# Optimization experiments

Measured on AMD Instinct MI355X. Metric: run time of the kernel, lower is better.

Reference implementation:

```python
import jax, jax.numpy as jnp
import numpy as np

B = 500_000
D = 128
L = 4


def setup_inputs() -> dict:
    key = jax.random.key(0)
    k1, k2 = jax.random.split(key)
    inputs = jax.random.normal(k1, (B, D), dtype=jnp.float32)
    # xavier_normal for [D,1] slices: std = sqrt(2/(D+1))
    std = float(np.sqrt(2.0 / (D + 1)))
    kernels = jax.random.normal(k2, (L, D, 1), dtype=jnp.float32) * std
    biases = jnp.zeros((L, D, 1), dtype=jnp.float32)
    return {"inputs": inputs, "kernels": kernels, "biases": biases}


def reference(inputs, kernels, biases):
    # inputs: [B, D]; kernels/biases: [L, D, 1]
    x0 = inputs  # [B, D]
    xl = x0
    for i in range(kernels.shape[0]):
        w = kernels[i, :, 0]  # [D]
        b = biases[i, :, 0]   # [D]
        xl_w = jnp.einsum('bd,d->b', xl, w)  # [B], scalar per sample
        xl = x0 * xl_w[:, None] + b + xl     # rank-1 cross + bias + residual
    return xl
```

## Files before the change

kernel.cpp:

```cpp
#include <hip/hip_runtime.h>


#define CN_D 128
#define CN_L 4

__global__ __launch_bounds__(256) void crossnet_kernel(
    const float* __restrict__ inputs,
    const float* __restrict__ kernels,
    const float* __restrict__ biases,
    float* __restrict__ out,
    int nrows)
{
    const int lane = threadIdx.x & 31;
    const int row_in_blk = threadIdx.x >> 5;
    const int rows_per_blk = blockDim.x >> 5;

    float4 w4[CN_L], b4[CN_L];
#pragma unroll
    for (int i = 0; i < CN_L; ++i) {
        w4[i] = ((const float4*)(kernels + i * CN_D))[lane];
        b4[i] = ((const float4*)(biases + i * CN_D))[lane];
    }

    for (long long row = (long long)blockIdx.x * rows_per_blk + row_in_blk;
         row < nrows;
         row += (long long)gridDim.x * rows_per_blk)
    {
        const float4* xp = (const float4*)(inputs + row * CN_D);
        float4 x = xp[lane];
        float4 xl = x;

#pragma unroll
        for (int i = 0; i < CN_L; ++i) {
            float p = xl.x * w4[i].x + xl.y * w4[i].y
                    + xl.z * w4[i].z + xl.w * w4[i].w;
            p += __shfl_xor(p, 1);
            p += __shfl_xor(p, 2);
            p += __shfl_xor(p, 4);
            p += __shfl_xor(p, 8);
            p += __shfl_xor(p, 16);
            xl.x = fmaf(x.x, p, xl.x + b4[i].x);
            xl.y = fmaf(x.y, p, xl.y + b4[i].y);
            xl.z = fmaf(x.z, p, xl.z + b4[i].z);
            xl.w = fmaf(x.w, p, xl.w + b4[i].w);
        }

        float4* op = (float4*)(out + row * CN_D);
        op[lane] = xl;
    }
}

extern "C" void kernel_launch(void* const* d_in, const int* in_sizes, int n_in,
                              void* d_out, int out_size, void* d_ws, size_t ws_size,
                              hipStream_t stream) {
    const float* inputs  = (const float*)d_in[0];
    const float* kernels = (const float*)d_in[1];
    const float* biases  = (const float*)d_in[2];
    float* out = (float*)d_out;

    const int nrows = in_sizes[0] / CN_D;

    const int block = 256;
    const int grid  = 4096;

    crossnet_kernel<<<grid, block, 0, stream>>>(inputs, kernels, biases, out, nrows);
}
```

Before: 418.1 us.

## Collapse cross layers algebraically, process two rows per group, nontemporal stores

Rewrites the recurrence as xl = a*x0 + beta. The scalar a comes from four independent dot products of x0 with each layer weight, combined with precomputed bias-weight terms c[i]. This removes the serial dependency between the per-layer shuffle reductions. Each 32-lane group now processes two rows per iteration to add independent loads and shuffles for latency hiding, and outputs use nontemporal stores. The algebra relies on xl staying a scalar multiple of x0 plus a constant vector, and may change floating-point rounding slightly.

```diff
diff --git a/kernel.cpp b/kernel.cpp
--- a/kernel.cpp
+++ b/kernel.cpp
@@ -3,6 +3,8 @@
 
 #define CN_D 128
 #define CN_L 4
+
+typedef float fvec4 __attribute__((ext_vector_type(4)));
 
 __global__ __launch_bounds__(256) void crossnet_kernel(
     const float* __restrict__ inputs,
@@ -12,8 +14,8 @@
     int nrows)
 {
     const int lane = threadIdx.x & 31;
-    const int row_in_blk = threadIdx.x >> 5;
-    const int rows_per_blk = blockDim.x >> 5;
+    const int grp_in_blk = threadIdx.x >> 5;
+    const int grps_per_blk = blockDim.x >> 5;
 
     float4 w4[CN_L], b4[CN_L];
 #pragma unroll
@@ -22,31 +24,84 @@
         b4[i] = ((const float4*)(biases + i * CN_D))[lane];
     }
 
-    for (long long row = (long long)blockIdx.x * rows_per_blk + row_in_blk;
-         row < nrows;
-         row += (long long)gridDim.x * rows_per_blk)
+    float c[CN_L];
+    float4 beta = make_float4(0.f, 0.f, 0.f, 0.f);
+#pragma unroll
+    for (int i = 0; i < CN_L; ++i) {
+        float p = beta.x * w4[i].x + beta.y * w4[i].y
+                + beta.z * w4[i].z + beta.w * w4[i].w;
+        p += __shfl_xor(p, 1);
+        p += __shfl_xor(p, 2);
+        p += __shfl_xor(p, 4);
+        p += __shfl_xor(p, 8);
+        p += __shfl_xor(p, 16);
+        c[i] = p;
+        beta.x += b4[i].x; beta.y += b4[i].y;
+        beta.z += b4[i].z; beta.w += b4[i].w;
+    }
+
+    const long long gsz = (long long)gridDim.x * grps_per_blk;
+
+    for (long long rowA = (long long)blockIdx.x * grps_per_blk + grp_in_blk;
+         rowA < nrows;
+         rowA += 2 * gsz)
     {
-        const float4* xp = (const float4*)(inputs + row * CN_D);
-        float4 x = xp[lane];
-        float4 xl = x;
+        const long long rowB = rowA + gsz;
+        const bool hasB = (rowB < nrows);
+        const long long rB = hasB ? rowB : rowA;
 
-#pragma unroll
-        for (int i = 0; i < CN_L; ++i) {
-            float p = xl.x * w4[i].x + xl.y * w4[i].y
-                    + xl.z * w4[i].z + xl.w * w4[i].w;
-            p += __shfl_xor(p, 1);
-            p += __shfl_xor(p, 2);
-            p += __shfl_xor(p, 4);
-            p += __shfl_xor(p, 8);
-            p += __shfl_xor(p, 16);
-            xl.x = fmaf(x.x, p, xl.x + b4[i].x);
-            xl.y = fmaf(x.y, p, xl.y + b4[i].y);
-            xl.z = fmaf(x.z, p, xl.z + b4[i].z);
-            xl.w = fmaf(x.w, p, xl.w + b4[i].w);
-        }
+        float4 xA = ((const float4*)(inputs + rowA * CN_D))[lane];
+        float4 xB = ((const float4*)(inputs + rB  * CN_D))[lane];
 
-        float4* op = (float4*)(out + row * CN_D);
-        op[lane] = xl;
+        float dA0 = xA.x*w4[0].x + xA.y*w4[0].y + xA.z*w4[0].z + xA.w*w4[0].w;
+        float dA1 = xA.x*w4[1].x + xA.y*w4[1].y + xA.z*w4[1].z + xA.w*w4[1].w;
+        float dA2 = xA.x*w4[2].x + xA.y*w4[2].y + xA.z*w4[2].z + xA.w*w4[2].w;
+        float dA3 = xA.x*w4[3].x + xA.y*w4[3].y + xA.z*w4[3].z + xA.w*w4[3].w;
+        float dB0 = xB.x*w4[0].x + xB.y*w4[0].y + xB.z*w4[0].z + xB.w*w4[0].w;
+        float dB1 = xB.x*w4[1].x + xB.y*w4[1].y + xB.z*w4[1].z + xB.w*w4[1].w;
+        float dB2 = xB.x*w4[2].x + xB.y*w4[2].y + xB.z*w4[2].z + xB.w*w4[2].w;
+        float dB3 = xB.x*w4[3].x + xB.y*w4[3].y + xB.z*w4[3].z + xB.w*w4[3].w;
+
+        dA0 += __shfl_xor(dA0, 1);  dA1 += __shfl_xor(dA1, 1);
+        dA2 += __shfl_xor(dA2, 1);  dA3 += __shfl_xor(dA3, 1);
+        dB0 += __shfl_xor(dB0, 1);  dB1 += __shfl_xor(dB1, 1);
+        dB2 += __shfl_xor(dB2, 1);  dB3 += __shfl_xor(dB3, 1);
+
+        dA0 += __shfl_xor(dA0, 2);  dA1 += __shfl_xor(dA1, 2);
+        dA2 += __shfl_xor(dA2, 2);  dA3 += __shfl_xor(dA3, 2);
+        dB0 += __shfl_xor(dB0, 2);  dB1 += __shfl_xor(dB1, 2);
+        dB2 += __shfl_xor(dB2, 2);  dB3 += __shfl_xor(dB3, 2);
+
+        dA0 += __shfl_xor(dA0, 4);  dA1 += __shfl_xor(dA1, 4);
+        dA2 += __shfl_xor(dA2, 4);  dA3 += __shfl_xor(dA3, 4);
+        dB0 += __shfl_xor(dB0, 4);  dB1 += __shfl_xor(dB1, 4);
+        dB2 += __shfl_xor(dB2, 4);  dB3 += __shfl_xor(dB3, 4);
+
+        dA0 += __shfl_xor(dA0, 8);  dA1 += __shfl_xor(dA1, 8);
+        dA2 += __shfl_xor(dA2, 8);  dA3 += __shfl_xor(dA3, 8);
+        dB0 += __shfl_xor(dB0, 8);  dB1 += __shfl_xor(dB1, 8);
+        dB2 += __shfl_xor(dB2, 8);  dB3 += __shfl_xor(dB3, 8);
+
+        dA0 += __shfl_xor(dA0, 16); dA1 += __shfl_xor(dA1, 16);
+        dA2 += __shfl_xor(dA2, 16); dA3 += __shfl_xor(dA3, 16);
+        dB0 += __shfl_xor(dB0, 16); dB1 += __shfl_xor(dB1, 16);
+        dB2 += __shfl_xor(dB2, 16); dB3 += __shfl_xor(dB3, 16);
+
+        float aA = 1.f, aB = 1.f;
+        aA = fmaf(aA, dA0 + 1.f, c[0]);  aB = fmaf(aB, dB0 + 1.f, c[0]);
+        aA = fmaf(aA, dA1 + 1.f, c[1]);  aB = fmaf(aB, dB1 + 1.f, c[1]);
+        aA = fmaf(aA, dA2 + 1.f, c[2]);  aB = fmaf(aB, dB2 + 1.f, c[2]);
+        aA = fmaf(aA, dA3 + 1.f, c[3]);  aB = fmaf(aB, dB3 + 1.f, c[3]);
+
+        fvec4 oA, oB;
+        oA.x = fmaf(aA, xA.x, beta.x);  oA.y = fmaf(aA, xA.y, beta.y);
+        oA.z = fmaf(aA, xA.z, beta.z);  oA.w = fmaf(aA, xA.w, beta.w);
+        oB.x = fmaf(aB, xB.x, beta.x);  oB.y = fmaf(aB, xB.y, beta.y);
+        oB.z = fmaf(aB, xB.z, beta.z);  oB.w = fmaf(aB, xB.w, beta.w);
+
+        __builtin_nontemporal_store(oA, (fvec4*)(out + rowA * CN_D) + lane);
+        if (hasB)
+            __builtin_nontemporal_store(oB, (fvec4*)(out + rowB * CN_D) + lane);
     }
 }
 
```

Result: slower. 439.6 us (+5.1%).

## Collapse cross layers into one scalar recurrence with DPP reductions and prefetch

Applied to the files above, without the earlier changes.

Rewrites the per-row computation using the fact that every layer's output equals a scalar times x0 plus a cumulative bias. The four dot products with x0 are computed independently, and constants from the bias terms are precomputed per thread. This removes the serial dependency between layer reductions. The kernel also uses 16-lane groups with DPP row reductions in place of shuffles and prefetches the next row. The workload is memory-bound, so the gain depends mainly on whether the prefetch and the different access pattern help bandwidth.

```diff
diff --git a/kernel.cpp b/kernel.cpp
--- a/kernel.cpp
+++ b/kernel.cpp
@@ -3,6 +3,19 @@
 
 #define CN_D 128
 #define CN_L 4
+
+template <int CTRL>
+__device__ __forceinline__ float dpp_radd(float x) {
+    int t = __builtin_amdgcn_update_dpp(0, __float_as_int(x), CTRL, 0xF, 0xF, true);
+    return x + __int_as_float(t);
+}
+__device__ __forceinline__ float row16_allreduce(float x) {
+    x = dpp_radd<0xB1>(x);
+    x = dpp_radd<0x4E>(x);
+    x = dpp_radd<0x124>(x);
+    x = dpp_radd<0x128>(x);
+    return x;
+}
 
 __global__ __launch_bounds__(256) void crossnet_kernel(
     const float* __restrict__ inputs,
@@ -11,42 +24,90 @@
     float* __restrict__ out,
     int nrows)
 {
-    const int lane = threadIdx.x & 31;
-    const int row_in_blk = threadIdx.x >> 5;
-    const int rows_per_blk = blockDim.x >> 5;
+    const int lane = threadIdx.x & 15;
+    const int grp  = threadIdx.x >> 4;
+    const int gpb  = blockDim.x >> 4;
 
-    float4 w4[CN_L], b4[CN_L];
+    float4 wlo[CN_L], whi[CN_L];
 #pragma unroll
     for (int i = 0; i < CN_L; ++i) {
-        w4[i] = ((const float4*)(kernels + i * CN_D))[lane];
-        b4[i] = ((const float4*)(biases + i * CN_D))[lane];
+        wlo[i] = ((const float4*)(kernels + i * CN_D))[lane];
+        whi[i] = ((const float4*)(kernels + i * CN_D))[lane + 16];
     }
 
-    for (long long row = (long long)blockIdx.x * rows_per_blk + row_in_blk;
-         row < nrows;
-         row += (long long)gridDim.x * rows_per_blk)
-    {
-        const float4* xp = (const float4*)(inputs + row * CN_D);
-        float4 x = xp[lane];
-        float4 xl = x;
+    float c[CN_L];
+    float4 blo = make_float4(0.f, 0.f, 0.f, 0.f);
+    float4 bhi = make_float4(0.f, 0.f, 0.f, 0.f);
+#pragma unroll
+    for (int i = 0; i < CN_L; ++i) {
+        float p = blo.x*wlo[i].x + blo.y*wlo[i].y + blo.z*wlo[i].z + blo.w*wlo[i].w
+                + bhi.x*whi[i].x + bhi.y*whi[i].y + bhi.z*whi[i].z + bhi.w*whi[i].w;
+        c[i] = row16_allreduce(p);
+        float4 t;
+        t = ((const float4*)(biases + i * CN_D))[lane];
+        blo.x += t.x; blo.y += t.y; blo.z += t.z; blo.w += t.w;
+        t = ((const float4*)(biases + i * CN_D))[lane + 16];
+        bhi.x += t.x; bhi.y += t.y; bhi.z += t.z; bhi.w += t.w;
+    }
 
-#pragma unroll
-        for (int i = 0; i < CN_L; ++i) {
-            float p = xl.x * w4[i].x + xl.y * w4[i].y
-                    + xl.z * w4[i].z + xl.w * w4[i].w;
-            p += __shfl_xor(p, 1);
-            p += __shfl_xor(p, 2);
-            p += __shfl_xor(p, 4);
-            p += __shfl_xor(p, 8);
-            p += __shfl_xor(p, 16);
-            xl.x = fmaf(x.x, p, xl.x + b4[i].x);
-            xl.y = fmaf(x.y, p, xl.y + b4[i].y);
-            xl.z = fmaf(x.z, p, xl.z + b4[i].z);
-            xl.w = fmaf(x.w, p, xl.w + b4[i].w);
-        }
+    const int stride = gridDim.x * gpb;
+    int row = blockIdx.x * gpb + grp;
+    if (row >= nrows) return;
 
-        float4* op = (float4*)(out + row * CN_D);
-        op[lane] = xl;
+    const float4* __restrict__ in4  = (const float4*)inputs;
+    float4* __restrict__       out4 = (float4*)out;
+
+    float4 xlo = in4[row * 32 + lane];
+    float4 xhi = in4[row * 32 + lane + 16];
+
+    while (true) {
+        const int rnext = row + stride;
+        const bool hasN = rnext < nrows;
+        const int rn = hasN ? rnext : row;
+        float4 nlo = in4[rn * 32 + lane];
+        float4 nhi = in4[rn * 32 + lane + 16];
+
+        float d0, d1, d2, d3;
+        d0 = xlo.x * wlo[0].x;                 d1 = xlo.x * wlo[1].x;
+        d2 = xlo.x * wlo[2].x;                 d3 = xlo.x * wlo[3].x;
+        d0 = fmaf(xlo.y, wlo[0].y, d0);        d1 = fmaf(xlo.y, wlo[1].y, d1);
+        d2 = fmaf(xlo.y, wlo[2].y, d2);        d3 = fmaf(xlo.y, wlo[3].y, d3);
+        d0 = fmaf(xlo.z, wlo[0].z, d0);        d1 = fmaf(xlo.z, wlo[1].z, d1);
+        d2 = fmaf(xlo.z, wlo[2].z, d2);        d3 = fmaf(xlo.z, wlo[3].z, d3);
+        d0 = fmaf(xlo.w, wlo[0].w, d0);        d1 = fmaf(xlo.w, wlo[1].w, d1);
+        d2 = fmaf(xlo.w, wlo[2].w, d2);        d3 = fmaf(xlo.w, wlo[3].w, d3);
+        d0 = fmaf(xhi.x, whi[0].x, d0);        d1 = fmaf(xhi.x, whi[1].x, d1);
+        d2 = fmaf(xhi.x, whi[2].x, d2);        d3 = fmaf(xhi.x, whi[3].x, d3);
+        d0 = fmaf(xhi.y, whi[0].y, d0);        d1 = fmaf(xhi.y, whi[1].y, d1);
+        d2 = fmaf(xhi.y, whi[2].y, d2);        d3 = fmaf(xhi.y, whi[3].y, d3);
+        d0 = fmaf(xhi.z, whi[0].z, d0);        d1 = fmaf(xhi.z, whi[1].z, d1);
+        d2 = fmaf(xhi.z, whi[2].z, d2);        d3 = fmaf(xhi.z, whi[3].z, d3);
+        d0 = fmaf(xhi.w, whi[0].w, d0);        d1 = fmaf(xhi.w, whi[1].w, d1);
+        d2 = fmaf(xhi.w, whi[2].w, d2);        d3 = fmaf(xhi.w, whi[3].w, d3);
+
+        d0 = row16_allreduce(d0);
+        d1 = row16_allreduce(d1);
+        d2 = row16_allreduce(d2);
+        d3 = row16_allreduce(d3);
+
+        float a = d0 + 1.f + c[0];
+        a = fmaf(a, d1 + 1.f, c[1]);
+        a = fmaf(a, d2 + 1.f, c[2]);
+        a = fmaf(a, d3 + 1.f, c[3]);
+
+        float4 olo, ohi;
+        olo.x = fmaf(a, xlo.x, blo.x);  olo.y = fmaf(a, xlo.y, blo.y);
+        olo.z = fmaf(a, xlo.z, blo.z);  olo.w = fmaf(a, xlo.w, blo.w);
+        ohi.x = fmaf(a, xhi.x, bhi.x);  ohi.y = fmaf(a, xhi.y, bhi.y);
+        ohi.z = fmaf(a, xhi.z, bhi.z);  ohi.w = fmaf(a, xhi.w, bhi.w);
+
+        out4[row * 32 + lane]      = olo;
+        out4[row * 32 + lane + 16] = ohi;
+
+        if (!hasN) break;
+        row = rnext;
+        xlo = nlo;
+        xhi = nhi;
     }
 }
 
```

Result: no change. 419.7 us (+0.4%).
